# Kernel tuning notes

Measured on AMD Instinct MI355X. Metric: run time of the kernel, lower is better.

## Reference

```python
import jax, jax.numpy as jnp
import numpy as np

B, T, DIM = 2, 2048, 2048
H, KVH = 32, 8
HD = DIM // H            # 64
Q_PER_KV = H // KVH      # 4
ROPE_THETA = 10000.0


def _rope_tables(T, hd, dtype=jnp.float32):
    inv_freq = 1.0 / (ROPE_THETA ** (jnp.arange(0, hd, 2, dtype=jnp.float32) / hd))  # [hd/2]
    ang = jnp.arange(T, dtype=jnp.float32)[:, None] * inv_freq[None, :]              # [T, hd/2]
    return jnp.cos(ang).astype(dtype), jnp.sin(ang).astype(dtype)


def _apply_rope(x, cos, sin):
    # x: [B, T, h, hd]; cos/sin: [T, hd/2] -> complex multiply on (even, odd) pairs
    B_, T_, h, hd = x.shape
    xr = x.reshape(B_, T_, h, hd // 2, 2)
    xe, xo = xr[..., 0], xr[..., 1]
    c = cos[None, :, None, :]
    s = sin[None, :, None, :]
    re = xe * c - xo * s
    ro = xe * s + xo * c
    return jnp.stack([re, ro], axis=-1).reshape(B_, T_, h, hd)


def setup_inputs() -> dict:
    key = jax.random.key(0)
    kx, kq, kk, kv, ko = jax.random.split(key, 5)
    std = 0.02
    x = jax.random.normal(kx, (B, T, DIM), dtype=jnp.float32)
    wq = jax.random.normal(kq, (DIM, H * HD), dtype=jnp.float32) * std
    wk = jax.random.normal(kk, (DIM, KVH * HD), dtype=jnp.float32) * std
    wv = jax.random.normal(kv, (DIM, KVH * HD), dtype=jnp.float32) * std
    wo = jax.random.normal(ko, (H * HD, DIM), dtype=jnp.float32) * std
    freqs_cos, freqs_sin = _rope_tables(T, HD)
    causal = jnp.tril(jnp.ones((T, T), dtype=bool))
    mask = jnp.where(causal, 0.0, -jnp.inf).astype(jnp.float32)[None, None]  # [1,1,T,T]
    return {"x": x, "wq": wq, "wk": wk, "wv": wv, "wo": wo,
            "freqs_cos": freqs_cos, "freqs_sin": freqs_sin, "mask": mask}


def reference(x, wq, wk, wv, wo, freqs_cos, freqs_sin, mask):
    B_, T_, _ = x.shape
    q = (x @ wq).reshape(B_, T_, H, HD)
    k = (x @ wk).reshape(B_, T_, KVH, HD)
    v = (x @ wv).reshape(B_, T_, KVH, HD)
    q = _apply_rope(q, freqs_cos, freqs_sin)
    k = _apply_rope(k, freqs_cos, freqs_sin)
    # GQA: repeat_interleave KV heads along head dim
    k = jnp.repeat(k, Q_PER_KV, axis=2)
    v = jnp.repeat(v, Q_PER_KV, axis=2)
    q = q.transpose(0, 2, 1, 3)  # [B,H,T,hd]
    k = k.transpose(0, 2, 1, 3)
    v = v.transpose(0, 2, 1, 3)
    scale = HD ** -0.5
    scores = jnp.einsum('bhqd,bhkd->bhqk', q, k) * scale + mask
    probs = jax.nn.softmax(scores.astype(jnp.float32), axis=-1).astype(q.dtype)
    out = jnp.einsum('bhqk,bhkd->bhqd', probs, v)
    out = out.transpose(0, 2, 1, 3).reshape(B_, T_, H * HD)
    return out @ wo
```

## Files before the change

kernel.cpp:

```cpp
#include <hip/hip_runtime.h>
#include <stdint.h>

typedef __bf16 bf16;
typedef __attribute__((ext_vector_type(8))) __bf16 bf16x8;
typedef __attribute__((ext_vector_type(4))) __bf16 bf16x4;
typedef __attribute__((ext_vector_type(4))) float f32x4;
typedef __attribute__((ext_vector_type(16))) float f32x16;
typedef __attribute__((ext_vector_type(4))) unsigned short us4;

constexpr int B_   = 2;
constexpr int T_   = 2048;
constexpr int DIM_ = 2048;
constexpr int H_   = 32;
constexpr int KVH_ = 8;
constexpr int HD_  = 64;
constexpr int BT_ROWS = B_ * T_;
constexpr int NQKV = H_*HD_ + 2*KVH_*HD_;
constexpr int KOFF = H_*HD_;
constexpr int VOFF = H_*HD_ + KVH_*HD_;

#define DEV __device__ __forceinline__

DEV void gload16(const void* g, void* l) {
  __builtin_amdgcn_global_load_lds((const __attribute__((address_space(1))) void*)g,
                                   (__attribute__((address_space(3))) void*)l,
                                   16, 0, 0);
}

__global__ void prep_kernel(const float* __restrict__ x,
                            const float* __restrict__ wq, const float* __restrict__ wk,
                            const float* __restrict__ wv, const float* __restrict__ wo,
                            const float* __restrict__ fc, const float* __restrict__ fs,
                            bf16* __restrict__ xb, bf16* __restrict__ wT,
                            bf16* __restrict__ woT,
                            float* __restrict__ fcT, float* __restrict__ fsT) {
  const int id = blockIdx.x;
  const int tid = threadIdx.y * 32 + threadIdx.x;
  if (id < 8192) {
    int gid = id * 256 + tid;
    float4 f = ((const float4*)x)[gid];
    bf16x4 o;
    o[0] = (bf16)f.x; o[1] = (bf16)f.y; o[2] = (bf16)f.z; o[3] = (bf16)f.w;
    ((bf16x4*)xb)[gid] = o;
    return;
  }
  __shared__ float tile[32][33];
  int td = id - 8192;
  int tx = threadIdx.x, ty = threadIdx.y;
  if (td < 10240) {
    const float* in; bf16* out; int C, bid;
    if (td < 4096)      { in = wq; out = wT;               C = 2048; bid = td; }
    else if (td < 5120) { in = wk; out = wT + 2048*2048;   C = 512;  bid = td - 4096; }
    else if (td < 6144) { in = wv; out = wT + 2560*2048;   C = 512;  bid = td - 5120; }
    else                { in = wo; out = woT;              C = 2048; bid = td - 6144; }
    const int R = 2048;
    int ct = C / 32;
    int bx = bid % ct, by = bid / ct;
#pragma unroll
    for (int i = ty; i < 32; i += 8)
      tile[i][tx] = in[(by*32 + i) * C + bx*32 + tx];
    __syncthreads();
#pragma unroll
    for (int i = ty; i < 32; i += 8)
      out[(bx*32 + i) * R + by*32 + tx] = (bf16)tile[tx][i];
  } else {
    int tt = td - 10240;
    const float* in = (tt >= 64) ? fs : fc;
    float* outf = (tt >= 64) ? fsT : fcT;
    int bid = tt & 63;
#pragma unroll
    for (int i = ty; i < 32; i += 8)
      tile[i][tx] = in[(bid*32 + i) * 32 + tx];
    __syncthreads();
#pragma unroll
    for (int i = ty; i < 32; i += 8)
      outf[i * 2048 + bid*32 + tx] = tile[tx][i];
  }
}

template<int MODE>
__global__ __launch_bounds__(256, MODE == 1 ? 3 : 2)
void gemm_bt(const bf16* __restrict__ A, const bf16* __restrict__ BTm,
             void* __restrict__ Cv, int M, int N, int K,
             const float* __restrict__ fcT, const float* __restrict__ fsT,
             bf16* __restrict__ vt) {
  __shared__ __align__(16) bf16 As[128 * 64];
  __shared__ __align__(16) bf16 Bs[128 * 64];
  const int nbn = N >> 7;
  const int bm = blockIdx.x / nbn, bn = blockIdx.x % nbn;
  const int tid = threadIdx.x;
  const int w = tid >> 6, l = tid & 63;
  const int wr = w >> 1, wc = w & 1;
  const int lr = l & 31;
  const int hi = l >> 5;
  const int crow = l >> 3;
  const int cch  = (l & 7) ^ crow;

  f32x16 acc[2][2];
#pragma unroll
  for (int i = 0; i < 2; ++i)
#pragma unroll
    for (int j = 0; j < 2; ++j) acc[i][j] = 0.f;

  const bf16* ap[4];
  const bf16* bp[4];
#pragma unroll
  for (int i = 0; i < 4; ++i) {
    int row = (w*4 + i) * 8 + crow;
    ap[i] = A   + (long)(bm*128 + row) * K + cch*8;
    bp[i] = BTm + (long)(bn*128 + row) * K + cch*8;
  }
  int aoff[4][2], boff[4][2];
#pragma unroll
  for (int ks = 0; ks < 4; ++ks)
#pragma unroll
    for (int i = 0; i < 2; ++i) {
      int arow = wr*64 + i*32 + lr;
      int brow = wc*64 + i*32 + lr;
      aoff[ks][i] = arow*64 + (((2*ks + hi) ^ (arow & 7)) << 3);
      boff[ks][i] = brow*64 + (((2*ks + hi) ^ (brow & 7)) << 3);
    }

  for (int k0 = 0; k0 < K; k0 += 64) {
#pragma unroll
    for (int i = 0; i < 4; ++i) {
      gload16(ap[i], &As[(w*4 + i) * 512]);
      gload16(bp[i], &Bs[(w*4 + i) * 512]);
      ap[i] += 64; bp[i] += 64;
    }
    __syncthreads();
#pragma unroll
    for (int ks = 0; ks < 4; ++ks) {
      bf16x8 af[2], bfr[2];
#pragma unroll
      for (int i = 0; i < 2; ++i) af[i]  = *(const bf16x8*)&As[aoff[ks][i]];
#pragma unroll
      for (int j = 0; j < 2; ++j) bfr[j] = *(const bf16x8*)&Bs[boff[ks][j]];
#pragma unroll
      for (int i = 0; i < 2; ++i)
#pragma unroll
        for (int j = 0; j < 2; ++j)
          acc[i][j] = __builtin_amdgcn_mfma_f32_32x32x16_bf16(af[i], bfr[j], acc[i][j], 0, 0, 0);
    }
    __syncthreads();
  }

  const int row0 = bm*128 + wr*64, col0 = bn*128 + wc*64;
  if (MODE == 0) {
#pragma unroll
    for (int i = 0; i < 2; ++i)
#pragma unroll
      for (int j = 0; j < 2; ++j)
#pragma unroll
        for (int reg = 0; reg < 16; ++reg) {
          int rr = row0 + i*32 + (reg & 3) + 8*(reg >> 2) + 4*hi;
          int cc = col0 + j*32 + lr;
          ((float*)Cv)[(long)rr * N + cc] = acc[i][j][reg];
        }
  } else {
    if (col0 < VOFF) {
      const float sgn = (lr & 1) ? 1.f : -1.f;
#pragma unroll
      for (int i = 0; i < 2; ++i) {
        const int tb0 = ((row0 + i*32) & (T_ - 1)) + 4*hi;
#pragma unroll
        for (int j = 0; j < 2; ++j) {
          const int cc = col0 + j*32 + lr;
          const float qsc = (col0 + j*32 < KOFF) ? 0.18033688f : 1.0f;
          const int p0 = (cc & 63) >> 1;
          const float* fct = fcT + p0*2048 + tb0;
          const float* fst = fsT + p0*2048 + tb0;
#pragma unroll
          for (int q = 0; q < 4; ++q) {
            float4 c4 = *(const float4*)(fct + 8*q);
            float4 s4 = *(const float4*)(fst + 8*q);
#pragma unroll
            for (int r = 0; r < 4; ++r) {
              float v = acc[i][j][q*4 + r];
              float other = __shfl_xor(v, 1);
              float cse = (&c4.x)[r], sse = (&s4.x)[r];
              float out = fmaf(sgn * other, sse, v * cse) * qsc;
              const int rr = row0 + i*32 + r + 8*q + 4*hi;
              ((bf16*)Cv)[(long)rr * N + cc] = (bf16)out;
            }
          }
        }
      }
    } else {
      const int bglob = row0 >> 11;
#pragma unroll
      for (int i = 0; i < 2; ++i)
#pragma unroll
        for (int j = 0; j < 2; ++j) {
          const int vo = col0 + j*32 + lr - VOFF;
          const long vbase = (long)((bglob*KVH_ + (vo >> 6))*HD_ + (vo & 63)) * T_;
#pragma unroll
          for (int q = 0; q < 4; ++q) {
            bf16x4 pk;
#pragma unroll
            for (int r = 0; r < 4; ++r) pk[r] = (bf16)acc[i][j][q*4 + r];
            const int t = ((row0 + i*32) & (T_ - 1)) + 8*q + 4*hi;
            *(bf16x4*)&vt[vbase + t] = pk;
          }
        }
    }
  }
}

__global__ __launch_bounds__(256, 4)
void attn_kernel(const bf16* __restrict__ qkvb, const bf16* __restrict__ vt,
                 bf16* __restrict__ att) {
  const int o = blockIdx.x;
  const int xcd = o & 7, s = o >> 3;
  const int bh = xcd * 8 + (s & 7);
  const int qt = 15 - (s >> 3);
  const int h = bh & 31, b = bh >> 5;
  const int kvh = h >> 2;
  const int tid = threadIdx.x, w = tid >> 6, l = tid & 63;
  const int ln = l & 15, g = l >> 4;

  __shared__ __align__(16) bf16 Ks[2][4096];
  __shared__ __align__(16) bf16 Vs[2][4096];

  const int srow = tid >> 3;
  const int sch  = (tid & 7) ^ (srow & 7);
  const bf16* kg = qkvb + (long)(b*T_ + srow) * NQKV + KOFF + kvh*HD_ + sch*8;
  const bf16* vg = vt + (long)((b*KVH_ + kvh) * HD_ + srow) * T_ + sch*8;
  const int ldsoff = tid * 8;

  const int qrel0 = (w & 1)*32 + ln;
  const int qrel1 = qrel0 + 16;

  bf16x8 onesf;
  {
    const bf16 ov = (ln == 0) ? (bf16)1.0f : (bf16)0.0f;
#pragma unroll
    for (int i = 0; i < 8; ++i) onesf[i] = ov;
  }

  const int qbase = qt * 128;
  const int nt = qt * 2 + 2;
  const int myNt = qt*2 + 1 + (w >> 1);

  const int q0 = qbase + w*32;
  const long qb0 = (long)(b*T_ + q0 + ln) * NQKV + h*HD_;
  const long qb1 = (long)(b*T_ + q0 + 16 + ln) * NQKV + h*HD_;
  bf16x8 qf0a = *(const bf16x8*)&qkvb[qb0 + g*8];
  bf16x8 qf0b = *(const bf16x8*)&qkvb[qb0 + 32 + g*8];
  bf16x8 qf1a = *(const bf16x8*)&qkvb[qb1 + g*8];
  bf16x8 qf1b = *(const bf16x8*)&qkvb[qb1 + 32 + g*8];

  f32x4 oacc0[4], oacc1[4], osum0, osum1;
#pragma unroll
  for (int d = 0; d < 4; ++d) { oacc0[d] = 0.f; oacc1[d] = 0.f; }
  osum0 = 0.f; osum1 = 0.f;

  gload16(kg, &Ks[0][ldsoff]);
  gload16(kg + (long)32*NQKV, &Ks[0][ldsoff + 2048]);
  gload16(vg, &Vs[0][ldsoff]);
  gload16(vg + (long)32*T_, &Vs[0][ldsoff + 2048]);
  __syncthreads();

  int cur = 0;
  for (int kt = 0; kt < nt; ++kt) {
    if (kt + 1 < nt) {
      const int k1 = (kt + 1) * 64;
      gload16(kg + (long)k1 * NQKV,        &Ks[cur^1][ldsoff]);
      gload16(kg + (long)(k1+32) * NQKV,   &Ks[cur^1][ldsoff + 2048]);
      gload16(vg + k1,                     &Vs[cur^1][ldsoff]);
      gload16(vg + (long)32*T_ + k1,       &Vs[cur^1][ldsoff + 2048]);
    }
    if (kt < myNt) {
      f32x4 sv0[4], sv1[4];
      __builtin_amdgcn_s_setprio(1);
#pragma unroll
      for (int c = 0; c < 4; ++c) {
        const int krow = c*16 + ln, sw = krow & 7;
        bf16x8 kf0 = *(const bf16x8*)&Ks[cur][krow*64 + (( g    ^ sw) << 3)];
        bf16x8 kf1 = *(const bf16x8*)&Ks[cur][krow*64 + (((g+4) ^ sw) << 3)];
        f32x4 z0 = 0.f, z1 = 0.f;
        z0     = __builtin_amdgcn_mfma_f32_16x16x32_bf16(kf0, qf0a, z0, 0, 0, 0);
        sv0[c] = __builtin_amdgcn_mfma_f32_16x16x32_bf16(kf1, qf0b, z0, 0, 0, 0);
        z1     = __builtin_amdgcn_mfma_f32_16x16x32_bf16(kf0, qf1a, z1, 0, 0, 0);
        sv1[c] = __builtin_amdgcn_mfma_f32_16x16x32_bf16(kf1, qf1b, z1, 0, 0, 0);
      }
      __builtin_amdgcn_s_setprio(0);

      if (kt == myNt - 1) {
#pragma unroll
        for (int c = 0; c < 4; ++c)
#pragma unroll
          for (int r = 0; r < 4; ++r) {
            const int krel = c*16 + g*4 + r;
            sv0[c][r] += (krel > qrel0) ? -1e38f : 0.f;
            sv1[c][r] += (krel > qrel1) ? -1e38f : 0.f;
          }
      }

#pragma unroll
      for (int c = 0; c < 4; ++c)
#pragma unroll
        for (int r = 0; r < 4; ++r) {
          sv0[c][r] = exp2f(sv0[c][r]);
          sv1[c][r] = exp2f(sv1[c][r]);
        }

      bf16x8 pa0a, pa0b, pa1a, pa1b;
      {
        unsigned p0,p1,p2,p3,p4,p5,p6,p7;
        asm("v_cvt_pk_bf16_f32 %0, %1, %2" : "=v"(p0) : "v"(sv0[0][0]), "v"(sv0[0][1]));
        asm("v_cvt_pk_bf16_f32 %0, %1, %2" : "=v"(p1) : "v"(sv0[0][2]), "v"(sv0[0][3]));
        asm("v_cvt_pk_bf16_f32 %0, %1, %2" : "=v"(p2) : "v"(sv0[1][0]), "v"(sv0[1][1]));
        asm("v_cvt_pk_bf16_f32 %0, %1, %2" : "=v"(p3) : "v"(sv0[1][2]), "v"(sv0[1][3]));
        asm("v_cvt_pk_bf16_f32 %0, %1, %2" : "=v"(p4) : "v"(sv0[2][0]), "v"(sv0[2][1]));
        asm("v_cvt_pk_bf16_f32 %0, %1, %2" : "=v"(p5) : "v"(sv0[2][2]), "v"(sv0[2][3]));
        asm("v_cvt_pk_bf16_f32 %0, %1, %2" : "=v"(p6) : "v"(sv0[3][0]), "v"(sv0[3][1]));
        asm("v_cvt_pk_bf16_f32 %0, %1, %2" : "=v"(p7) : "v"(sv0[3][2]), "v"(sv0[3][3]));
        asm("v_permlane32_swap_b32 %0, %1" : "+v"(p0), "+v"(p2));
        asm("v_permlane32_swap_b32 %0, %1" : "+v"(p1), "+v"(p3));
        asm("v_permlane16_swap_b32 %0, %1" : "+v"(p0), "+v"(p2));
        asm("v_permlane16_swap_b32 %0, %1" : "+v"(p1), "+v"(p3));
        asm("v_permlane32_swap_b32 %0, %1" : "+v"(p4), "+v"(p6));
        asm("v_permlane32_swap_b32 %0, %1" : "+v"(p5), "+v"(p7));
        asm("v_permlane16_swap_b32 %0, %1" : "+v"(p4), "+v"(p6));
        asm("v_permlane16_swap_b32 %0, %1" : "+v"(p5), "+v"(p7));
        union { unsigned u[4]; bf16x8 v; } ua, ub;
        ua.u[0]=p0; ua.u[1]=p1; ua.u[2]=p2; ua.u[3]=p3; pa0a = ua.v;
        ub.u[0]=p4; ub.u[1]=p5; ub.u[2]=p6; ub.u[3]=p7; pa0b = ub.v;
      }
      {
        unsigned p0,p1,p2,p3,p4,p5,p6,p7;
        asm("v_cvt_pk_bf16_f32 %0, %1, %2" : "=v"(p0) : "v"(sv1[0][0]), "v"(sv1[0][1]));
        asm("v_cvt_pk_bf16_f32 %0, %1, %2" : "=v"(p1) : "v"(sv1[0][2]), "v"(sv1[0][3]));
        asm("v_cvt_pk_bf16_f32 %0, %1, %2" : "=v"(p2) : "v"(sv1[1][0]), "v"(sv1[1][1]));
        asm("v_cvt_pk_bf16_f32 %0, %1, %2" : "=v"(p3) : "v"(sv1[1][2]), "v"(sv1[1][3]));
        asm("v_cvt_pk_bf16_f32 %0, %1, %2" : "=v"(p4) : "v"(sv1[2][0]), "v"(sv1[2][1]));
        asm("v_cvt_pk_bf16_f32 %0, %1, %2" : "=v"(p5) : "v"(sv1[2][2]), "v"(sv1[2][3]));
        asm("v_cvt_pk_bf16_f32 %0, %1, %2" : "=v"(p6) : "v"(sv1[3][0]), "v"(sv1[3][1]));
        asm("v_cvt_pk_bf16_f32 %0, %1, %2" : "=v"(p7) : "v"(sv1[3][2]), "v"(sv1[3][3]));
        asm("v_permlane32_swap_b32 %0, %1" : "+v"(p0), "+v"(p2));
        asm("v_permlane32_swap_b32 %0, %1" : "+v"(p1), "+v"(p3));
        asm("v_permlane16_swap_b32 %0, %1" : "+v"(p0), "+v"(p2));
        asm("v_permlane16_swap_b32 %0, %1" : "+v"(p1), "+v"(p3));
        asm("v_permlane32_swap_b32 %0, %1" : "+v"(p4), "+v"(p6));
        asm("v_permlane32_swap_b32 %0, %1" : "+v"(p5), "+v"(p7));
        asm("v_permlane16_swap_b32 %0, %1" : "+v"(p4), "+v"(p6));
        asm("v_permlane16_swap_b32 %0, %1" : "+v"(p5), "+v"(p7));
        union { unsigned u[4]; bf16x8 v; } ua, ub;
        ua.u[0]=p0; ua.u[1]=p1; ua.u[2]=p2; ua.u[3]=p3; pa1a = ua.v;
        ub.u[0]=p4; ub.u[1]=p5; ub.u[2]=p6; ub.u[3]=p7; pa1b = ub.v;
      }

      __builtin_amdgcn_s_setprio(1);
#pragma unroll
      for (int d = 0; d < 4; ++d) {
        const int vrow = d*16 + ln, sw = vrow & 7;
        bf16x8 vf0 = *(const bf16x8*)&Vs[cur][vrow*64 + (( g    ^ sw) << 3)];
        bf16x8 vf1 = *(const bf16x8*)&Vs[cur][vrow*64 + (((g+4) ^ sw) << 3)];
        oacc0[d] = __builtin_amdgcn_mfma_f32_16x16x32_bf16(vf0, pa0a, oacc0[d], 0, 0, 0);
        oacc0[d] = __builtin_amdgcn_mfma_f32_16x16x32_bf16(vf1, pa0b, oacc0[d], 0, 0, 0);
        oacc1[d] = __builtin_amdgcn_mfma_f32_16x16x32_bf16(vf0, pa1a, oacc1[d], 0, 0, 0);
        oacc1[d] = __builtin_amdgcn_mfma_f32_16x16x32_bf16(vf1, pa1b, oacc1[d], 0, 0, 0);
      }
      osum0 = __builtin_amdgcn_mfma_f32_16x16x32_bf16(onesf, pa0a, osum0, 0, 0, 0);
      osum0 = __builtin_amdgcn_mfma_f32_16x16x32_bf16(onesf, pa0b, osum0, 0, 0, 0);
      osum1 = __builtin_amdgcn_mfma_f32_16x16x32_bf16(onesf, pa1a, osum1, 0, 0, 0);
      osum1 = __builtin_amdgcn_mfma_f32_16x16x32_bf16(onesf, pa1b, osum1, 0, 0, 0);
      __builtin_amdgcn_s_setprio(0);
    }
    __syncthreads();
    cur ^= 1;
  }

  {
    const float lsum = __shfl(osum0[0], ln);
    const float inv = 1.f / lsum;
    const long ob = (long)(b*T_ + q0 + ln) * DIM_ + h*HD_;
#pragma unroll
    for (int d = 0; d < 4; ++d) {
      bf16x4 ov;
#pragma unroll
      for (int r = 0; r < 4; ++r) ov[r] = (bf16)(oacc0[d][r] * inv);
      *(bf16x4*)&att[ob + d*16 + g*4] = ov;
    }
  }
  {
    const float lsum = __shfl(osum1[0], ln);
    const float inv = 1.f / lsum;
    const long ob = (long)(b*T_ + q0 + 16 + ln) * DIM_ + h*HD_;
#pragma unroll
    for (int d = 0; d < 4; ++d) {
      bf16x4 ov;
#pragma unroll
      for (int r = 0; r < 4; ++r) ov[r] = (bf16)(oacc1[d][r] * inv);
      *(bf16x4*)&att[ob + d*16 + g*4] = ov;
    }
  }
}

extern "C" void kernel_launch(void* const* d_in, const int* in_sizes, int n_in,
                              void* d_out, int out_size, void* d_ws, size_t ws_size,
                              hipStream_t stream) {
  const float* x  = (const float*)d_in[0];
  const float* wq = (const float*)d_in[1];
  const float* wk = (const float*)d_in[2];
  const float* wv = (const float*)d_in[3];
  const float* wo = (const float*)d_in[4];
  const float* fc = (const float*)d_in[5];
  const float* fs = (const float*)d_in[6];

  char* ws = (char*)d_ws;
  bf16* xb   = (bf16*)(ws);
  bf16* wT   = (bf16*)(ws + 16777216);
  bf16* woT  = (bf16*)(ws + 29360128);
  bf16* qkvb = (bf16*)(ws + 37748736);
  bf16* vtb  = (bf16*)(ws + 62914560);
  bf16* att  = (bf16*)(ws + 67108864);
  float* fcT = (float*)(ws + 67108864);
  float* fsT = fcT + 32*2048;

  dim3 tb(32, 8);
  prep_kernel<<<18560, tb, 0, stream>>>(x, wq, wk, wv, wo, fc, fs, xb, wT, woT, fcT, fsT);

  gemm_bt<1><<<(BT_ROWS/128) * (NQKV/128), 256, 0, stream>>>(
      xb, wT, qkvb, BT_ROWS, NQKV, DIM_, fcT, fsT, vtb);

  attn_kernel<<<1024, 256, 0, stream>>>(qkvb, vtb, att);

  gemm_bt<0><<<(BT_ROWS/128) * (DIM_/128), 256, 0, stream>>>(
      att, woT, d_out, BT_ROWS, DIM_, DIM_, nullptr, nullptr, nullptr);
}
```

Measured before the change: 190.4 us.

## Software-pipeline attention loop: run PV of previous tile alongside QK of current

Restructures the attention inner loop so each iteration runs the P·V MFMAs for the previous key tile together with the Q·K MFMAs for the current tile, then does exp and bf16 packing. A third V buffer in shared memory keeps the previous tile's V alive, and an epilogue after the loop finishes the last P·V. The goal is to let the matrix unit overlap with the exp/convert/permlane work and shorten the dependency chain within each iteration. The cost is more LDS per block, which may reduce occupancy, and P fragments stay live across iterations, which raises register pressure.

```diff
diff --git a/kernel.cpp b/kernel.cpp
--- a/kernel.cpp
+++ b/kernel.cpp
@@ -220,7 +220,7 @@
   const int ln = l & 15, g = l >> 4;
 
   __shared__ __align__(16) bf16 Ks[2][4096];
-  __shared__ __align__(16) bf16 Vs[2][4096];
+  __shared__ __align__(16) bf16 Vs[3][4096];
 
   const int srow = tid >> 3;
   const int sch  = (tid & 7) ^ (srow & 7);
@@ -255,37 +255,61 @@
   for (int d = 0; d < 4; ++d) { oacc0[d] = 0.f; oacc1[d] = 0.f; }
   osum0 = 0.f; osum1 = 0.f;
 
+  bf16x8 pa0a, pa0b, pa1a, pa1b;
+
   gload16(kg, &Ks[0][ldsoff]);
   gload16(kg + (long)32*NQKV, &Ks[0][ldsoff + 2048]);
   gload16(vg, &Vs[0][ldsoff]);
   gload16(vg + (long)32*T_, &Vs[0][ldsoff + 2048]);
   __syncthreads();
 
-  int cur = 0;
+  int vprev = 2, vcur = 0, vnext = 1;
   for (int kt = 0; kt < nt; ++kt) {
+    const int kcur = kt & 1;
     if (kt + 1 < nt) {
       const int k1 = (kt + 1) * 64;
-      gload16(kg + (long)k1 * NQKV,        &Ks[cur^1][ldsoff]);
-      gload16(kg + (long)(k1+32) * NQKV,   &Ks[cur^1][ldsoff + 2048]);
-      gload16(vg + k1,                     &Vs[cur^1][ldsoff]);
-      gload16(vg + (long)32*T_ + k1,       &Vs[cur^1][ldsoff + 2048]);
-    }
-    if (kt < myNt) {
-      f32x4 sv0[4], sv1[4];
-      __builtin_amdgcn_s_setprio(1);
+      gload16(kg + (long)k1 * NQKV,        &Ks[kcur^1][ldsoff]);
+      gload16(kg + (long)(k1+32) * NQKV,   &Ks[kcur^1][ldsoff + 2048]);
+      gload16(vg + k1,                     &Vs[vnext][ldsoff]);
+      gload16(vg + (long)32*T_ + k1,       &Vs[vnext][ldsoff + 2048]);
+    }
+    const bool doPV = (kt >= 1) && (kt - 1 < myNt);
+    const bool doQK = kt < myNt;
+
+    f32x4 sv0[4], sv1[4];
+    __builtin_amdgcn_s_setprio(1);
+    if (doPV) {
+#pragma unroll
+      for (int d = 0; d < 4; ++d) {
+        const int vrow = d*16 + ln, sw = vrow & 7;
+        bf16x8 vf0 = *(const bf16x8*)&Vs[vprev][vrow*64 + (( g    ^ sw) << 3)];
+        bf16x8 vf1 = *(const bf16x8*)&Vs[vprev][vrow*64 + (((g+4) ^ sw) << 3)];
+        oacc0[d] = __builtin_amdgcn_mfma_f32_16x16x32_bf16(vf0, pa0a, oacc0[d], 0, 0, 0);
+        oacc0[d] = __builtin_amdgcn_mfma_f32_16x16x32_bf16(vf1, pa0b, oacc0[d], 0, 0, 0);
+        oacc1[d] = __builtin_amdgcn_mfma_f32_16x16x32_bf16(vf0, pa1a, oacc1[d], 0, 0, 0);
+        oacc1[d] = __builtin_amdgcn_mfma_f32_16x16x32_bf16(vf1, pa1b, oacc1[d], 0, 0, 0);
+      }
+      osum0 = __builtin_amdgcn_mfma_f32_16x16x32_bf16(onesf, pa0a, osum0, 0, 0, 0);
+      osum0 = __builtin_amdgcn_mfma_f32_16x16x32_bf16(onesf, pa0b, osum0, 0, 0, 0);
+      osum1 = __builtin_amdgcn_mfma_f32_16x16x32_bf16(onesf, pa1a, osum1, 0, 0, 0);
+      osum1 = __builtin_amdgcn_mfma_f32_16x16x32_bf16(onesf, pa1b, osum1, 0, 0, 0);
+    }
+    if (doQK) {
 #pragma unroll
       for (int c = 0; c < 4; ++c) {
         const int krow = c*16 + ln, sw = krow & 7;
-        bf16x8 kf0 = *(const bf16x8*)&Ks[cur][krow*64 + (( g    ^ sw) << 3)];
-        bf16x8 kf1 = *(const bf16x8*)&Ks[cur][krow*64 + (((g+4) ^ sw) << 3)];
+        bf16x8 kf0 = *(const bf16x8*)&Ks[kcur][krow*64 + (( g    ^ sw) << 3)];
+        bf16x8 kf1 = *(const bf16x8*)&Ks[kcur][krow*64 + (((g+4) ^ sw) << 3)];
         f32x4 z0 = 0.f, z1 = 0.f;
         z0     = __builtin_amdgcn_mfma_f32_16x16x32_bf16(kf0, qf0a, z0, 0, 0, 0);
         sv0[c] = __builtin_amdgcn_mfma_f32_16x16x32_bf16(kf1, qf0b, z0, 0, 0, 0);
         z1     = __builtin_amdgcn_mfma_f32_16x16x32_bf16(kf0, qf1a, z1, 0, 0, 0);
         sv1[c] = __builtin_amdgcn_mfma_f32_16x16x32_bf16(kf1, qf1b, z1, 0, 0, 0);
       }
-      __builtin_amdgcn_s_setprio(0);
-
+    }
+    __builtin_amdgcn_s_setprio(0);
+
+    if (doQK) {
       if (kt == myNt - 1) {
 #pragma unroll
         for (int c = 0; c < 4; ++c)
@@ -296,7 +320,6 @@
             sv1[c][r] += (krel > qrel1) ? -1e38f : 0.f;
           }
       }
-
 #pragma unroll
       for (int c = 0; c < 4; ++c)
 #pragma unroll
@@ -304,8 +327,6 @@
           sv0[c][r] = exp2f(sv0[c][r]);
           sv1[c][r] = exp2f(sv1[c][r]);
         }
-
-      bf16x8 pa0a, pa0b, pa1a, pa1b;
       {
         unsigned p0,p1,p2,p3,p4,p5,p6,p7;
         asm("v_cvt_pk_bf16_f32 %0, %1, %2" : "=v"(p0) : "v"(sv0[0][0]), "v"(sv0[0][1]));
@@ -350,26 +371,26 @@
         ua.u[0]=p0; ua.u[1]=p1; ua.u[2]=p2; ua.u[3]=p3; pa1a = ua.v;
         ub.u[0]=p4; ub.u[1]=p5; ub.u[2]=p6; ub.u[3]=p7; pa1b = ub.v;
       }
-
-      __builtin_amdgcn_s_setprio(1);
-#pragma unroll
-      for (int d = 0; d < 4; ++d) {
-        const int vrow = d*16 + ln, sw = vrow & 7;
-        bf16x8 vf0 = *(const bf16x8*)&Vs[cur][vrow*64 + (( g    ^ sw) << 3)];
-        bf16x8 vf1 = *(const bf16x8*)&Vs[cur][vrow*64 + (((g+4) ^ sw) << 3)];
-        oacc0[d] = __builtin_amdgcn_mfma_f32_16x16x32_bf16(vf0, pa0a, oacc0[d], 0, 0, 0);
-        oacc0[d] = __builtin_amdgcn_mfma_f32_16x16x32_bf16(vf1, pa0b, oacc0[d], 0, 0, 0);
-        oacc1[d] = __builtin_amdgcn_mfma_f32_16x16x32_bf16(vf0, pa1a, oacc1[d], 0, 0, 0);
-        oacc1[d] = __builtin_amdgcn_mfma_f32_16x16x32_bf16(vf1, pa1b, oacc1[d], 0, 0, 0);
-      }
-      osum0 = __builtin_amdgcn_mfma_f32_16x16x32_bf16(onesf, pa0a, osum0, 0, 0, 0);
-      osum0 = __builtin_amdgcn_mfma_f32_16x16x32_bf16(onesf, pa0b, osum0, 0, 0, 0);
-      osum1 = __builtin_amdgcn_mfma_f32_16x16x32_bf16(onesf, pa1a, osum1, 0, 0, 0);
-      osum1 = __builtin_amdgcn_mfma_f32_16x16x32_bf16(onesf, pa1b, osum1, 0, 0, 0);
-      __builtin_amdgcn_s_setprio(0);
     }
     __syncthreads();
-    cur ^= 1;
+    const int t = vprev; vprev = vcur; vcur = vnext; vnext = t;
+  }
+
+  if (nt - 1 < myNt) {
+#pragma unroll
+    for (int d = 0; d < 4; ++d) {
+      const int vrow = d*16 + ln, sw = vrow & 7;
+      bf16x8 vf0 = *(const bf16x8*)&Vs[vprev][vrow*64 + (( g    ^ sw) << 3)];
+      bf16x8 vf1 = *(const bf16x8*)&Vs[vprev][vrow*64 + (((g+4) ^ sw) << 3)];
+      oacc0[d] = __builtin_amdgcn_mfma_f32_16x16x32_bf16(vf0, pa0a, oacc0[d], 0, 0, 0);
+      oacc0[d] = __builtin_amdgcn_mfma_f32_16x16x32_bf16(vf1, pa0b, oacc0[d], 0, 0, 0);
+      oacc1[d] = __builtin_amdgcn_mfma_f32_16x16x32_bf16(vf0, pa1a, oacc1[d], 0, 0, 0);
+      oacc1[d] = __builtin_amdgcn_mfma_f32_16x16x32_bf16(vf1, pa1b, oacc1[d], 0, 0, 0);
+    }
+    osum0 = __builtin_amdgcn_mfma_f32_16x16x32_bf16(onesf, pa0a, osum0, 0, 0, 0);
+    osum0 = __builtin_amdgcn_mfma_f32_16x16x32_bf16(onesf, pa0b, osum0, 0, 0, 0);
+    osum1 = __builtin_amdgcn_mfma_f32_16x16x32_bf16(onesf, pa1a, osum1, 0, 0, 0);
+    osum1 = __builtin_amdgcn_mfma_f32_16x16x32_bf16(onesf, pa1b, osum1, 0, 0, 0);
   }
 
   {
```

Result: slower. 194.6 us (+2.2%).
